# Performance work log

Hardware: AMD Instinct MI355X
Metric: run time of the kernel (lower is better)

## Reference

```python
import jax, jax.numpy as jnp
import numpy as np

SR = 24000
N_FFT = 1024
N_MELS = 128
FMIN = 0.0
LPC_ORDER = 4
REPEAT = 256
F0 = 40.0
CLAMP = 1e-12
T_FRAMES = 16384


def _hz_to_mel(f):
    # librosa slaney scale
    f = np.asarray(f, dtype=np.float64)
    f_sp = 200.0 / 3
    min_log_hz = 1000.0
    min_log_mel = min_log_hz / f_sp
    logstep = np.log(6.4) / 27.0
    mels = f / f_sp
    log_t = f >= min_log_hz
    mels = np.where(log_t, min_log_mel + np.log(np.maximum(f, min_log_hz) / min_log_hz) / logstep, mels)
    return mels


def _mel_to_hz(m):
    m = np.asarray(m, dtype=np.float64)
    f_sp = 200.0 / 3
    min_log_hz = 1000.0
    min_log_mel = min_log_hz / f_sp
    logstep = np.log(6.4) / 27.0
    freqs = f_sp * m
    log_t = m >= min_log_mel
    freqs = np.where(log_t, min_log_hz * np.exp(logstep * (m - min_log_mel)), freqs)
    return freqs


def librosa_mel_fn(sr, n_fft, n_mels, fmin, fmax):
    if fmax is None:
        fmax = sr / 2.0
    fftfreqs = np.linspace(0.0, sr / 2.0, n_fft // 2 + 1)
    mel_f = _mel_to_hz(np.linspace(_hz_to_mel(fmin), _hz_to_mel(fmax), n_mels + 2))
    fdiff = np.diff(mel_f)
    ramps = mel_f[:, None] - fftfreqs[None, :]
    lower = -ramps[:-2] / fdiff[:-1, None]
    upper = ramps[2:] / fdiff[1:, None]
    weights = np.maximum(0.0, np.minimum(lower, upper))
    enorm = 2.0 / (mel_f[2 : n_mels + 2] - mel_f[:n_mels])  # slaney norm
    weights *= enorm[:, None]
    return weights.astype(np.float32)


def setup_inputs() -> dict:
    key = jax.random.key(0)
    mel = jax.random.normal(key, (1, N_MELS, T_FRAMES), dtype=jnp.float32)
    mel_basis = librosa_mel_fn(SR, N_FFT, N_MELS, FMIN, None)  # [128, 513]
    inv_mel_basis = jnp.asarray(np.linalg.pinv(mel_basis), dtype=jnp.float32)  # [513, 128]
    theta = (2.0 * np.pi * F0 / SR) ** 2
    lag_window = jnp.asarray(
        np.exp(-0.5 * theta * np.arange(LPC_ORDER + 1, dtype=np.float32) ** 2)[:, None],
        dtype=jnp.float32,
    )  # [lpc_order+1, 1]
    return {"mel": mel, "inv_mel_basis": inv_mel_basis, "lag_window": lag_window}


def _levinson_durbin(AC, n):
    # AC: [n+1, T] autocorrelation; returns LPC coeffs [n, T]
    E = AC[0]
    lp = []  # list of [T]
    for i in range(n):
        acc = AC[i + 1]
        for j in range(i):
            acc = acc + lp[j] * AC[i - j]
        ki = acc / E
        c = jnp.maximum(1.0 - ki * ki, 1e-5)
        E = E * c
        lp = [lp[j] - ki * lp[i - j - 1] for j in range(i)] + [-ki]
    return jnp.stack(lp, axis=0)  # [n, T]


def reference(mel, inv_mel_basis, lag_window):
    # mel: [1, n_mel, T]
    mel_lin = jnp.power(10.0, mel)
    linear = jnp.maximum(jnp.einsum("fm,bmt->bft", inv_mel_basis, mel_lin), CLAMP)  # [1, 513, T]
    power = linear ** 2
    flipped = jnp.flip(power, axis=1)[:, 1:-1, :]
    fft_power = jnp.concatenate([power, flipped], axis=1)  # [1, n_fft, T]
    auto_corr = jnp.fft.ifft(fft_power, axis=1).real[:, : LPC_ORDER + 1, :]  # [1, n+1, T]
    auto_corr = auto_corr * lag_window[None, :, :]
    lpc = _levinson_durbin(auto_corr[0], LPC_ORDER)[None]  # [1, n, T]
    lpc_ctrl = -jnp.flip(lpc, axis=1)
    lpc_ctrl = jnp.repeat(lpc_ctrl, REPEAT, axis=-1)  # [1, n, T*repeat]
    return lpc_ctrl
```

## Files before the change

### kernel.cpp

```cpp
#include <hip/hip_runtime.h>

#define T_FRAMES 16384
#define N_MELS 128
#define N_FREQ 513
#define FPB 32
#define BT 512
#define LOG2_10 3.3219280948873623f

typedef short bf16x8 __attribute__((ext_vector_type(8)));
typedef unsigned short u16x8 __attribute__((ext_vector_type(8)));
typedef float f32x4 __attribute__((ext_vector_type(4)));

__device__ __forceinline__ unsigned short f2bf(float x) {
  unsigned u = __float_as_uint(x);
  return (unsigned short)((u + 0x7FFFu + ((u >> 16) & 1u)) >> 16);
}
__device__ __forceinline__ float bf2f(unsigned short h) {
  return __uint_as_float(((unsigned)h) << 16);
}

__global__ __launch_bounds__(256) void build_bimg(
    const float* __restrict__ B, unsigned short* __restrict__ img) {
  int gid = blockIdx.x * 256 + threadIdx.x;
  int l  = gid & 63;
  int hl = (gid >> 6) & 1;
  int ks = (gid >> 7) & 3;
  int ft = (gid >> 9) & 3;
  int w  = gid >> 11;
  int f  = w * 64 + ft * 16 + (l & 15);
  int k0 = ks * 32 + (l >> 4) * 8;
  const float* src = B + f * N_MELS + k0;
  u16x8 o;
#pragma unroll
  for (int j = 0; j < 8; ++j) {
    float x = src[j];
    unsigned short hi = f2bf(x);
    o[j] = hl ? f2bf(x - bf2f(hi)) : hi;
  }
  *((u16x8*)img + gid) = o;
}

#define SM_X32T 0
#define SM_RED  0
#define SM_LP   5120
#define SM_XF   16896
#define SM_W    33280
#define SM_PV   43552
#define SM_SIZE 43712

__global__ __launch_bounds__(BT, 4) void mel2lpc_mfma(
    const float* __restrict__ mel,
    const float* __restrict__ B,
    const float* __restrict__ lag,
    const unsigned short* __restrict__ bimg,
    float* __restrict__ out)
{
  __shared__ __align__(16) char smem[SM_SIZE];
  float (*X32T)[132] = (float(*)[132])(smem + SM_X32T);
  short (*Xf)[512]   = (short(*)[512])(smem + SM_XF);
  float (*W_s)[513]  = (float(*)[513])(smem + SM_W);
  float (*red)[5][32] = (float(*)[5][32])(smem + SM_RED);
  float (*lp)[32]    = (float(*)[32])(smem + SM_LP);
  float* pv512       = (float*)(smem + SM_PV);

  const int tid = threadIdx.x;
  const int lane = tid & 63;
  const int w = __builtin_amdgcn_readfirstlane(tid >> 6);
  const int t0 = blockIdx.x * FPB;

#pragma unroll
  for (int k = 0; k < 5; ++k) {
    float lk = lag[k];
    for (int f = tid; f < N_FREQ; f += BT) {
      float cf = (f == 0 || f == N_FREQ - 1) ? (1.0f / 1024.0f) : (2.0f / 1024.0f);
      W_s[k][f] = lk * cf * cospif((float)(k * f) * (1.0f / 512.0f));
    }
  }
#pragma unroll
  for (int r = 0; r < 8; ++r) {
    int idx = r * BT + tid;
    int t = idx & 31;
    int m = idx >> 5;
    X32T[t][m] = exp2f(mel[m * T_FRAMES + t0 + t] * LOG2_10);
  }
  __syncthreads();

  if (tid < FPB) {
    const int t = tid;
    float s = 0.f;
    const float4* __restrict__ B512 = (const float4*)(B + 512 * N_MELS);
#pragma unroll
    for (int mi = 0; mi < 32; ++mi) {
      float4 b = B512[mi];
      float4 xv = *(const float4*)&X32T[t][mi * 4];
      s = fmaf(b.x, xv.x, s); s = fmaf(b.y, xv.y, s);
      s = fmaf(b.z, xv.z, s); s = fmaf(b.w, xv.w, s);
    }
    float lin = fmaxf(s, 1e-12f);
    pv512[t] = lin * lin;
  }
  {
    int tt = w >> 2, ks = w & 3;
    int t = tt * 16 + (lane & 15);
    int k0 = ks * 32 + (lane >> 4) * 8;
    float4 a0 = *(const float4*)&X32T[t][k0];
    float4 a1 = *(const float4*)&X32T[t][k0 + 4];
    float xs[8] = {a0.x, a0.y, a0.z, a0.w, a1.x, a1.y, a1.z, a1.w};
    u16x8 vh, vl;
#pragma unroll
    for (int j = 0; j < 8; ++j) {
      unsigned short hi = f2bf(xs[j]);
      vh[j] = hi;
      vl[j] = f2bf(xs[j] - bf2f(hi));
    }
    *(u16x8*)&Xf[w * 2][lane * 8] = vh;
    *(u16x8*)&Xf[w * 2 + 1][lane * 8] = vl;
  }
  __syncthreads();

  f32x4 acc[4][2];
#pragma unroll
  for (int ft = 0; ft < 4; ++ft)
#pragma unroll
    for (int tt = 0; tt < 2; ++tt) acc[ft][tt] = (f32x4){0.f, 0.f, 0.f, 0.f};

  const bf16x8* bfr = (const bf16x8*)bimg;
#pragma unroll
  for (int ks = 0; ks < 4; ++ks) {
    bf16x8 xh0 = *(const bf16x8*)&Xf[(0 * 4 + ks) * 2][lane * 8];
    bf16x8 xl0 = *(const bf16x8*)&Xf[(0 * 4 + ks) * 2 + 1][lane * 8];
    bf16x8 xh1 = *(const bf16x8*)&Xf[(1 * 4 + ks) * 2][lane * 8];
    bf16x8 xl1 = *(const bf16x8*)&Xf[(1 * 4 + ks) * 2 + 1][lane * 8];
#pragma unroll
    for (int ft = 0; ft < 4; ++ft) {
      int fr = ((w * 4 + ft) * 4 + ks) * 2;
      bf16x8 ah = bfr[fr * 64 + lane];
      bf16x8 al = bfr[(fr + 1) * 64 + lane];
      acc[ft][0] = __builtin_amdgcn_mfma_f32_16x16x32_bf16(ah, xh0, acc[ft][0], 0, 0, 0);
      acc[ft][0] = __builtin_amdgcn_mfma_f32_16x16x32_bf16(ah, xl0, acc[ft][0], 0, 0, 0);
      acc[ft][0] = __builtin_amdgcn_mfma_f32_16x16x32_bf16(al, xh0, acc[ft][0], 0, 0, 0);
      acc[ft][1] = __builtin_amdgcn_mfma_f32_16x16x32_bf16(ah, xh1, acc[ft][1], 0, 0, 0);
      acc[ft][1] = __builtin_amdgcn_mfma_f32_16x16x32_bf16(ah, xl1, acc[ft][1], 0, 0, 0);
      acc[ft][1] = __builtin_amdgcn_mfma_f32_16x16x32_bf16(al, xh1, acc[ft][1], 0, 0, 0);
    }
  }

  float pk[5][2];
#pragma unroll
  for (int k = 0; k < 5; ++k)
#pragma unroll
    for (int tt = 0; tt < 2; ++tt) pk[k][tt] = 0.f;

#pragma unroll
  for (int ft = 0; ft < 4; ++ft) {
#pragma unroll
    for (int j = 0; j < 4; ++j) {
      int f = w * 64 + ft * 16 + ((lane >> 4) << 2) + j;
      float w0 = W_s[0][f], w1 = W_s[1][f], w2 = W_s[2][f];
      float w3 = W_s[3][f], w4 = W_s[4][f];
#pragma unroll
      for (int tt = 0; tt < 2; ++tt) {
        float lin = fmaxf(acc[ft][tt][j], 1e-12f);
        float p = lin * lin;
        pk[0][tt] = fmaf(w0, p, pk[0][tt]);
        pk[1][tt] = fmaf(w1, p, pk[1][tt]);
        pk[2][tt] = fmaf(w2, p, pk[2][tt]);
        pk[3][tt] = fmaf(w3, p, pk[3][tt]);
        pk[4][tt] = fmaf(w4, p, pk[4][tt]);
      }
    }
  }
#pragma unroll
  for (int k = 0; k < 5; ++k)
#pragma unroll
    for (int tt = 0; tt < 2; ++tt) {
      float v = pk[k][tt];
      v += __shfl_xor(v, 16);
      v += __shfl_xor(v, 32);
      if (lane < 16) red[w][k][tt * 16 + lane] = v;
    }
  __syncthreads();

  if (tid < FPB) {
    const int t = tid;
    float ac[5];
#pragma unroll
    for (int k = 0; k < 5; ++k) {
      float s = 0.f;
#pragma unroll
      for (int w2 = 0; w2 < 8; ++w2) s += red[w2][k][t];
      ac[k] = s + W_s[k][512] * pv512[t];
    }

    float E = ac[0];
    float k0 = ac[1] / E;
    E *= fmaxf(1.0f - k0 * k0, 1e-5f);
    float l0 = -k0;

    float a1 = ac[2] + l0 * ac[1];
    float k1 = a1 / E;
    E *= fmaxf(1.0f - k1 * k1, 1e-5f);
    float m0 = l0 - k1 * l0;
    float m1 = -k1;

    float a2 = ac[3] + m0 * ac[2] + m1 * ac[1];
    float k2 = a2 / E;
    E *= fmaxf(1.0f - k2 * k2, 1e-5f);
    float n0 = m0 - k2 * m1;
    float n1 = m1 - k2 * m0;
    float n2 = -k2;

    float a3 = ac[4] + n0 * ac[3] + n1 * ac[2] + n2 * ac[1];
    float k3 = a3 / E;
    float o0 = n0 - k3 * n2;
    float o1 = n1 - k3 * n1;
    float o2 = n2 - k3 * n0;
    float o3 = -k3;

    lp[0][t] = -o3;
    lp[1][t] = -o2;
    lp[2][t] = -o1;
    lp[3][t] = -o0;
  }
  __syncthreads();

  float4* out4 = (float4*)out;
#pragma unroll
  for (int i = 0; i < 16; ++i) {
    int vid = i * BT + tid;
    int j = vid >> 11;
    int rem = vid & 2047;
    int tl = rem >> 6;
    float v = lp[j][tl];
    out4[(size_t)j * (T_FRAMES * 256 / 4) + (size_t)t0 * 64 + rem] =
        make_float4(v, v, v, v);
  }
}

extern "C" void kernel_launch(void* const* d_in, const int* in_sizes, int n_in,
                              void* d_out, int out_size, void* d_ws, size_t ws_size,
                              hipStream_t stream) {
  const float* mel = (const float*)d_in[0];
  const float* B   = (const float*)d_in[1];
  const float* lag = (const float*)d_in[2];
  unsigned short* bimg = (unsigned short*)d_ws;
  build_bimg<<<64, 256, 0, stream>>>(B, bimg);
  mel2lpc_mfma<<<T_FRAMES / FPB, BT, 0, stream>>>(mel, B, lag, bimg, (float*)d_out);
}
```

Measured before the change: 94.85 us.

## Halve block to 16 frames and 256 threads, restructure MFMA work split

```diff
diff --git a/kernel.cpp b/kernel.cpp
--- a/kernel.cpp
+++ b/kernel.cpp
@@ -3,8 +3,8 @@
 #define T_FRAMES 16384
 #define N_MELS 128
 #define N_FREQ 513
-#define FPB 32
-#define BT 512
+#define FPB 16
+#define BT 256
 #define LOG2_10 3.3219280948873623f
 
 typedef short bf16x8 __attribute__((ext_vector_type(8)));
@@ -40,14 +40,6 @@
   *((u16x8*)img + gid) = o;
 }
 
-#define SM_X32T 0
-#define SM_RED  0
-#define SM_LP   5120
-#define SM_XF   16896
-#define SM_W    33280
-#define SM_PV   43552
-#define SM_SIZE 43712
-
 __global__ __launch_bounds__(BT, 4) void mel2lpc_mfma(
     const float* __restrict__ mel,
     const float* __restrict__ B,
@@ -55,56 +47,50 @@
     const unsigned short* __restrict__ bimg,
     float* __restrict__ out)
 {
-  __shared__ __align__(16) char smem[SM_SIZE];
-  float (*X32T)[132] = (float(*)[132])(smem + SM_X32T);
-  short (*Xf)[512]   = (short(*)[512])(smem + SM_XF);
-  float (*W_s)[513]  = (float(*)[513])(smem + SM_W);
-  float (*red)[5][32] = (float(*)[5][32])(smem + SM_RED);
-  float (*lp)[32]    = (float(*)[32])(smem + SM_LP);
-  float* pv512       = (float*)(smem + SM_PV);
+  __shared__ float X16T[FPB][132];
+  __shared__ __align__(16) short Xf[8][512];
+  __shared__ float W_s[5][N_FREQ];
+  __shared__ float red[4][5][FPB];
+  __shared__ float lp[4][FPB];
+  __shared__ float pv512[FPB];
 
   const int tid = threadIdx.x;
   const int lane = tid & 63;
-  const int w = __builtin_amdgcn_readfirstlane(tid >> 6);
+  const int wv = __builtin_amdgcn_readfirstlane(tid >> 6);
   const int t0 = blockIdx.x * FPB;
 
-#pragma unroll
-  for (int k = 0; k < 5; ++k) {
-    float lk = lag[k];
-    for (int f = tid; f < N_FREQ; f += BT) {
-      float cf = (f == 0 || f == N_FREQ - 1) ? (1.0f / 1024.0f) : (2.0f / 1024.0f);
-      W_s[k][f] = lk * cf * cospif((float)(k * f) * (1.0f / 512.0f));
-    }
-  }
+  float mv[8];
 #pragma unroll
   for (int r = 0; r < 8; ++r) {
     int idx = r * BT + tid;
-    int t = idx & 31;
-    int m = idx >> 5;
-    X32T[t][m] = exp2f(mel[m * T_FRAMES + t0 + t] * LOG2_10);
-  }
-  __syncthreads();
-
-  if (tid < FPB) {
-    const int t = tid;
-    float s = 0.f;
-    const float4* __restrict__ B512 = (const float4*)(B + 512 * N_MELS);
-#pragma unroll
-    for (int mi = 0; mi < 32; ++mi) {
-      float4 b = B512[mi];
-      float4 xv = *(const float4*)&X32T[t][mi * 4];
-      s = fmaf(b.x, xv.x, s); s = fmaf(b.y, xv.y, s);
-      s = fmaf(b.z, xv.z, s); s = fmaf(b.w, xv.w, s);
-    }
-    float lin = fmaxf(s, 1e-12f);
-    pv512[t] = lin * lin;
-  }
+    int t = idx & 15;
+    int m = idx >> 4;
+    mv[r] = mel[m * T_FRAMES + t0 + t];
+  }
+  float la0 = lag[0], la1 = lag[1], la2 = lag[2], la3 = lag[3], la4 = lag[4];
+  for (int f = tid; f < N_FREQ; f += BT) {
+    float cf = (f == 0 || f == N_FREQ - 1) ? (1.0f / 1024.0f) : (2.0f / 1024.0f);
+    float ang = (float)f * (1.0f / 512.0f);
+    W_s[0][f] = la0 * cf;
+    W_s[1][f] = la1 * cf * cospif(ang);
+    W_s[2][f] = la2 * cf * cospif(2.0f * ang);
+    W_s[3][f] = la3 * cf * cospif(3.0f * ang);
+    W_s[4][f] = la4 * cf * cospif(4.0f * ang);
+  }
+#pragma unroll
+  for (int r = 0; r < 8; ++r) {
+    int idx = r * BT + tid;
+    int t = idx & 15;
+    int m = idx >> 4;
+    X16T[t][m] = exp2f(mv[r] * LOG2_10);
+  }
+  __syncthreads();
+
   {
-    int tt = w >> 2, ks = w & 3;
-    int t = tt * 16 + (lane & 15);
-    int k0 = ks * 32 + (lane >> 4) * 8;
-    float4 a0 = *(const float4*)&X32T[t][k0];
-    float4 a1 = *(const float4*)&X32T[t][k0 + 4];
+    int t = lane & 15;
+    int k0 = wv * 32 + (lane >> 4) * 8;
+    float4 a0 = *(const float4*)&X16T[t][k0];
+    float4 a1 = *(const float4*)&X16T[t][k0 + 4];
     float xs[8] = {a0.x, a0.y, a0.z, a0.w, a1.x, a1.y, a1.z, a1.w};
     u16x8 vh, vl;
 #pragma unroll
@@ -113,72 +99,74 @@
       vh[j] = hi;
       vl[j] = f2bf(xs[j] - bf2f(hi));
     }
-    *(u16x8*)&Xf[w * 2][lane * 8] = vh;
-    *(u16x8*)&Xf[w * 2 + 1][lane * 8] = vl;
-  }
-  __syncthreads();
-
-  f32x4 acc[4][2];
-#pragma unroll
-  for (int ft = 0; ft < 4; ++ft)
-#pragma unroll
-    for (int tt = 0; tt < 2; ++tt) acc[ft][tt] = (f32x4){0.f, 0.f, 0.f, 0.f};
+    *(u16x8*)&Xf[wv * 2][lane * 8] = vh;
+    *(u16x8*)&Xf[wv * 2 + 1][lane * 8] = vl;
+  }
+  if (wv == 0 && lane < FPB) {
+    const int t = lane;
+    float s = 0.f;
+    const float4* __restrict__ B512 = (const float4*)(B + 512 * N_MELS);
+#pragma unroll
+    for (int mi = 0; mi < 32; ++mi) {
+      float4 b = B512[mi];
+      float4 xv = *(const float4*)&X16T[t][mi * 4];
+      s = fmaf(b.x, xv.x, s); s = fmaf(b.y, xv.y, s);
+      s = fmaf(b.z, xv.z, s); s = fmaf(b.w, xv.w, s);
+    }
+    float lin = fmaxf(s, 1e-12f);
+    pv512[t] = lin * lin;
+  }
+  __syncthreads();
+
+  f32x4 acc[8];
+#pragma unroll
+  for (int ft = 0; ft < 8; ++ft) acc[ft] = (f32x4){0.f, 0.f, 0.f, 0.f};
 
   const bf16x8* bfr = (const bf16x8*)bimg;
 #pragma unroll
   for (int ks = 0; ks < 4; ++ks) {
-    bf16x8 xh0 = *(const bf16x8*)&Xf[(0 * 4 + ks) * 2][lane * 8];
-    bf16x8 xl0 = *(const bf16x8*)&Xf[(0 * 4 + ks) * 2 + 1][lane * 8];
-    bf16x8 xh1 = *(const bf16x8*)&Xf[(1 * 4 + ks) * 2][lane * 8];
-    bf16x8 xl1 = *(const bf16x8*)&Xf[(1 * 4 + ks) * 2 + 1][lane * 8];
-#pragma unroll
-    for (int ft = 0; ft < 4; ++ft) {
-      int fr = ((w * 4 + ft) * 4 + ks) * 2;
+    bf16x8 xh = *(const bf16x8*)&Xf[ks * 2][lane * 8];
+    bf16x8 xl = *(const bf16x8*)&Xf[ks * 2 + 1][lane * 8];
+#pragma unroll
+    for (int ft2 = 0; ft2 < 8; ++ft2) {
+      int w8 = wv * 2 + (ft2 >> 2);
+      int ftl = ft2 & 3;
+      int fr = ((w8 * 4 + ftl) * 4 + ks) * 2;
       bf16x8 ah = bfr[fr * 64 + lane];
       bf16x8 al = bfr[(fr + 1) * 64 + lane];
-      acc[ft][0] = __builtin_amdgcn_mfma_f32_16x16x32_bf16(ah, xh0, acc[ft][0], 0, 0, 0);
-      acc[ft][0] = __builtin_amdgcn_mfma_f32_16x16x32_bf16(ah, xl0, acc[ft][0], 0, 0, 0);
-      acc[ft][0] = __builtin_amdgcn_mfma_f32_16x16x32_bf16(al, xh0, acc[ft][0], 0, 0, 0);
-      acc[ft][1] = __builtin_amdgcn_mfma_f32_16x16x32_bf16(ah, xh1, acc[ft][1], 0, 0, 0);
-      acc[ft][1] = __builtin_amdgcn_mfma_f32_16x16x32_bf16(ah, xl1, acc[ft][1], 0, 0, 0);
-      acc[ft][1] = __builtin_amdgcn_mfma_f32_16x16x32_bf16(al, xh1, acc[ft][1], 0, 0, 0);
-    }
-  }
-
-  float pk[5][2];
-#pragma unroll
-  for (int k = 0; k < 5; ++k)
-#pragma unroll
-    for (int tt = 0; tt < 2; ++tt) pk[k][tt] = 0.f;
-
-#pragma unroll
-  for (int ft = 0; ft < 4; ++ft) {
+      acc[ft2] = __builtin_amdgcn_mfma_f32_16x16x32_bf16(ah, xh, acc[ft2], 0, 0, 0);
+      acc[ft2] = __builtin_amdgcn_mfma_f32_16x16x32_bf16(ah, xl, acc[ft2], 0, 0, 0);
+      acc[ft2] = __builtin_amdgcn_mfma_f32_16x16x32_bf16(al, xh, acc[ft2], 0, 0, 0);
+    }
+  }
+
+  float pk[5];
+#pragma unroll
+  for (int k = 0; k < 5; ++k) pk[k] = 0.f;
+
+#pragma unroll
+  for (int ft2 = 0; ft2 < 8; ++ft2) {
+    int w8 = wv * 2 + (ft2 >> 2);
+    int ftl = ft2 & 3;
 #pragma unroll
     for (int j = 0; j < 4; ++j) {
-      int f = w * 64 + ft * 16 + ((lane >> 4) << 2) + j;
-      float w0 = W_s[0][f], w1 = W_s[1][f], w2 = W_s[2][f];
-      float w3 = W_s[3][f], w4 = W_s[4][f];
-#pragma unroll
-      for (int tt = 0; tt < 2; ++tt) {
-        float lin = fmaxf(acc[ft][tt][j], 1e-12f);
-        float p = lin * lin;
-        pk[0][tt] = fmaf(w0, p, pk[0][tt]);
-        pk[1][tt] = fmaf(w1, p, pk[1][tt]);
-        pk[2][tt] = fmaf(w2, p, pk[2][tt]);
-        pk[3][tt] = fmaf(w3, p, pk[3][tt]);
-        pk[4][tt] = fmaf(w4, p, pk[4][tt]);
-      }
-    }
-  }
-#pragma unroll
-  for (int k = 0; k < 5; ++k)
-#pragma unroll
-    for (int tt = 0; tt < 2; ++tt) {
-      float v = pk[k][tt];
-      v += __shfl_xor(v, 16);
-      v += __shfl_xor(v, 32);
-      if (lane < 16) red[w][k][tt * 16 + lane] = v;
-    }
+      int f = w8 * 64 + ftl * 16 + ((lane >> 4) << 2) + j;
+      float lin = fmaxf(acc[ft2][j], 1e-12f);
+      float p = lin * lin;
+      pk[0] = fmaf(W_s[0][f], p, pk[0]);
+      pk[1] = fmaf(W_s[1][f], p, pk[1]);
+      pk[2] = fmaf(W_s[2][f], p, pk[2]);
+      pk[3] = fmaf(W_s[3][f], p, pk[3]);
+      pk[4] = fmaf(W_s[4][f], p, pk[4]);
+    }
+  }
+#pragma unroll
+  for (int k = 0; k < 5; ++k) {
+    float v = pk[k];
+    v += __shfl_xor(v, 16);
+    v += __shfl_xor(v, 32);
+    if (lane < FPB) red[wv][k][lane] = v;
+  }
   __syncthreads();
 
   if (tid < FPB) {
@@ -186,9 +174,7 @@
     float ac[5];
 #pragma unroll
     for (int k = 0; k < 5; ++k) {
-      float s = 0.f;
-#pragma unroll
-      for (int w2 = 0; w2 < 8; ++w2) s += red[w2][k][t];
+      float s = red[0][k][t] + red[1][k][t] + red[2][k][t] + red[3][k][t];
       ac[k] = s + W_s[k][512] * pv512[t];
     }
 
@@ -228,8 +214,8 @@
 #pragma unroll
   for (int i = 0; i < 16; ++i) {
     int vid = i * BT + tid;
-    int j = vid >> 11;
-    int rem = vid & 2047;
+    int j = vid >> 10;
+    int rem = vid & 1023;
     int tl = rem >> 6;
     float v = lp[j][tl];
     out4[(size_t)j * (T_FRAMES * 256 / 4) + (size_t)t0 * 64 + rem] =
```

Result: slower. 125.1 us (+31.9%).
